# Kernel tuning notes

Hardware: AMD Instinct MI355X
Metric: run time of the kernel (lower is better)

## Reference

```python
import jax, jax.numpy as jnp
import numpy as np

G = 8            # group_order
KS = 3           # kernel size
C1, O1 = 1, 16   # gconv1 channels
C2, O2 = 16, 32  # gconv2 channels
HW = 28
NUM_CLASSES = 10


def _bilinear_sample(img, px, py):
    # img: (O, I, K, K); px, py: (K, K) pixel coords; zero padding outside
    # (matches torch grid_sample bilinear, align_corners=False, padding_mode='zeros')
    K = img.shape[-1]
    x0 = jnp.floor(px); y0 = jnp.floor(py)
    wx = px - x0; wy = py - y0
    x0i = x0.astype(jnp.int32); y0i = y0.astype(jnp.int32)

    def gather(yi, xi):
        valid = (yi >= 0) & (yi < K) & (xi >= 0) & (xi < K)
        yc = jnp.clip(yi, 0, K - 1)
        xc = jnp.clip(xi, 0, K - 1)
        return img[:, :, yc, xc] * valid.astype(img.dtype)  # (O,I,K,K)

    return (gather(y0i, x0i) * (1 - wx) * (1 - wy)
            + gather(y0i, x0i + 1) * wx * (1 - wy)
            + gather(y0i + 1, x0i) * (1 - wx) * wy
            + gather(y0i + 1, x0i + 1) * wx * wy)


def _rotated_kernels(base, group_order):
    # Replicates F.affine_grid + F.grid_sample (align_corners=False) for each rotation k.
    K = base.shape[-1]
    coords = (2.0 * jnp.arange(K, dtype=base.dtype) + 1.0) / K - 1.0  # normalized centers
    xs, ys = jnp.meshgrid(coords, coords, indexing='xy')  # x along width, y along height

    def rot_k(k):
        theta = 2.0 * np.pi * k / group_order
        c, s = jnp.cos(theta), jnp.sin(theta)
        gx = c * xs - s * ys   # theta row [cos, -sin, 0]
        gy = s * xs + c * ys   # theta row [sin,  cos, 0]
        px = ((gx + 1.0) * K - 1.0) / 2.0  # unnormalize, align_corners=False
        py = ((gy + 1.0) * K - 1.0) / 2.0
        return _bilinear_sample(base, px, py)

    return jax.vmap(rot_k)(jnp.arange(group_order, dtype=base.dtype))  # (G,O,I,K,K)


def _conv2d(x, w, pad):
    return jax.lax.conv_general_dilated(
        x, w, window_strides=(1, 1), padding=[(pad, pad), (pad, pad)],
        dimension_numbers=('NCHW', 'OIHW', 'NCHW'))


def setup_inputs() -> dict:
    key = jax.random.key(0)
    k1, k2, k3, k4, k5 = jax.random.split(key, 5)
    x = jax.random.normal(k1, (512, C1, HW, HW), dtype=jnp.float32)
    base_weight = jax.random.normal(k2, (O1, C1, KS, KS), dtype=jnp.float32)
    w2 = jax.random.normal(k3, (O2, C2, G, KS, KS), dtype=jnp.float32) * 0.05
    fc_w = jax.random.normal(k4, (NUM_CLASSES, O2 * HW * HW), dtype=jnp.float32) * 0.01
    fc_b = jax.random.normal(k5, (NUM_CLASSES,), dtype=jnp.float32) * 0.01
    return {"x": x, "base_weight": base_weight, "w2": w2, "fc_w": fc_w, "fc_b": fc_b}


def reference(x, base_weight, w2, fc_w, fc_b):
    B = x.shape[0]
    # --- GroupConv2D: steerable rotated kernels, concat along out-channels (k-major) ---
    rk = _rotated_kernels(base_weight, G)           # (G, O1, C1, K, K)
    w1 = rk.reshape(G * O1, C1, KS, KS)
    h = _conv2d(x, w1, 1)                           # (B, G*O1, 28, 28)
    h = jax.nn.relu(h)                              # GroupReLU == plain ReLU

    # --- GroupToGroupConv: circulant structure fused into one conv ---
    # torch: out channel = g*O2 + o (cat dim=1), in channel = c*G + h_idx (view layout)
    g = jnp.arange(G)[:, None]
    hh = jnp.arange(G)[None, :]
    idx = (g - hh) % G                               # (G, G)
    Wc = w2[:, :, idx]                               # (O2, C2, G_g, G_h, K, K)
    Wbig = jnp.transpose(Wc, (2, 0, 1, 3, 4, 5)).reshape(G * O2, C2 * G, KS, KS)
    h2 = _conv2d(h, Wbig, 1)                         # (B, G*O2, 28, 28)
    h2 = jax.nn.relu(h2)

    # --- GroupPooling (mean over the *inner* factor of 8, as in the torch view) ---
    p = h2.reshape(B, (G * O2) // G, G, HW, HW).mean(axis=2)  # (B, 32, 28, 28)

    # --- fc ---
    flat = p.reshape(B, -1)
    return flat @ fc_w.T + fc_b
```

## Files before the change

### kernel.cpp

```cpp
#include <hip/hip_runtime.h>
#include <hip/hip_bf16.h>
#include <cstdint>

#define AS1 __attribute__((address_space(1)))
#define AS3 __attribute__((address_space(3)))

typedef __bf16 bf16x8 __attribute__((ext_vector_type(8)));
typedef float  f32x16 __attribute__((ext_vector_type(16)));

__device__ __forceinline__ void gld_lds16(const void* g, void* l) {
    __builtin_amdgcn_global_load_lds((const AS1 void*)g, (AS3 void*)l, 16, 0, 0);
}

__global__ void k_rot(const float* __restrict__ base, float* __restrict__ w1) {
    int m = threadIdx.x;
    int g = m >> 4, o = m & 15;
    float th = 6.28318530717958647692f * (float)g / 8.0f;
    float c = cosf(th), s = sinf(th);
    for (int i = 0; i < 3; ++i) {
        float ys = (2.0f * i + 1.0f) / 3.0f - 1.0f;
        for (int j = 0; j < 3; ++j) {
            float xs = (2.0f * j + 1.0f) / 3.0f - 1.0f;
            float gx = c * xs - s * ys;
            float gy = s * xs + c * ys;
            float px = ((gx + 1.0f) * 3.0f - 1.0f) * 0.5f;
            float py = ((gy + 1.0f) * 3.0f - 1.0f) * 0.5f;
            float x0 = floorf(px), y0 = floorf(py);
            float wx = px - x0, wy = py - y0;
            int x0i = (int)x0, y0i = (int)y0;
            auto gat = [&](int yi, int xi) -> float {
                bool v = (yi >= 0) && (yi < 3) && (xi >= 0) && (xi < 3);
                int yc = min(max(yi, 0), 2), xc = min(max(xi, 0), 2);
                return v ? base[o * 9 + yc * 3 + xc] : 0.0f;
            };
            w1[m * 9 + i * 3 + j] =
                  gat(y0i, x0i)         * (1.0f - wx) * (1.0f - wy)
                + gat(y0i, x0i + 1)     * wx          * (1.0f - wy)
                + gat(y0i + 1, x0i)     * (1.0f - wx) * wy
                + gat(y0i + 1, x0i + 1) * wx          * wy;
        }
    }
}

__global__ __launch_bounds__(256) void k_conv1(const float* __restrict__ x,
                                               const float* __restrict__ w1g,
                                               const float* __restrict__ w2,
                                               __hip_bfloat16* __restrict__ hl,
                                               __hip_bfloat16* __restrict__ A) {
    int tid = threadIdx.x;

    if (blockIdx.x < 1152) {
        int i = blockIdx.x * 256 + tid;
        int r = i / 1152, k = i - r * 1152;
        int g = r >> 5, o2 = r & 31;
        int kk = k >> 7, cch = k & 127;
        int ky = kk / 3, kx = kk - ky * 3;
        int c2 = cch >> 3, hh = cch & 7;
        int gi = (g - hh) & 7;
        float val = w2[((o2 * 16 + c2) * 8 + gi) * 9 + ky * 3 + kx];
        int half = cch >> 6, kt = cch & 63;
        int t = kk * 2 + half, ks2 = kt >> 4, hi2 = (kt >> 3) & 1, e = kt & 7;
        int mh = r >> 7, i2 = (r >> 5) & 3, row = r & 31;
        int aidx = ((((t * 2 + mh) * 16) + i2 * 4 + ks2) << 9) + ((hi2 << 5) + row) * 8 + e;
        A[aidx] = __float2bfloat16(val);
    }

    __shared__ float w1s[1152];
    for (int i = tid; i < 1152; i += 256) w1s[i] = w1g[i];
    __syncthreads();

    const int c0 = (tid & 15) * 8;
    float wreg[8][9];
#pragma unroll
    for (int cc = 0; cc < 8; ++cc)
#pragma unroll
        for (int k = 0; k < 9; ++k) wreg[cc][k] = w1s[(c0 + cc) * 9 + k];

    const int slot = tid >> 4;
    const int band = blockIdx.x % 15;
    const int b    = blockIdx.x / 15;
    const int yy   = band * 2 + (slot >> 3);
    const int xx0  = (slot & 7) * 4;

    const float* xb = x + b * 784;
    float xv[3][6];
#pragma unroll
    for (int t = 0; t < 3; ++t) {
        int sy = yy - 2 + t;
        bool syok = (sy >= 0) && (sy < 28);
#pragma unroll
        for (int u = 0; u < 6; ++u) {
            int sx = xx0 - 2 + u;
            bool ok = syok && (sx >= 0) && (sx < 28);
            xv[t][u] = ok ? xb[sy * 28 + sx] : 0.0f;
        }
    }

    float acc[4][8];
#pragma unroll
    for (int j = 0; j < 4; ++j)
#pragma unroll
        for (int cc = 0; cc < 8; ++cc) acc[j][cc] = 0.0f;

#pragma unroll
    for (int t = 0; t < 3; ++t)
#pragma unroll
        for (int u = 0; u < 3; ++u) {
#pragma unroll
            for (int j = 0; j < 4; ++j) {
                float xvv = xv[t][j + u];
#pragma unroll
                for (int cc = 0; cc < 8; ++cc)
                    acc[j][cc] += xvv * wreg[cc][t * 3 + u];
            }
        }

#pragma unroll
    for (int j = 0; j < 4; ++j) {
        int xx = xx0 + j;
        if (xx < 30) {
            bool interior = (yy >= 1) && (yy <= 28) && (xx >= 1) && (xx <= 28);
            union { __hip_bfloat16 h[8]; float4 f4; } u;
#pragma unroll
            for (int cc = 0; cc < 8; ++cc)
                u.h[cc] = __float2bfloat16(interior ? fmaxf(acc[j][cc], 0.0f) : 0.0f);
            int pi = b * 900 + yy * 30 + xx;
            *(float4*)(hl + (size_t)pi * 128 + c0) = u.f4;
        }
    }
}

__global__ __launch_bounds__(512, 2) void k_conv2(const __hip_bfloat16* __restrict__ A,
                                                  const __hip_bfloat16* __restrict__ hl,
                                                  __hip_bfloat16* __restrict__ p) {
    __shared__ __align__(16) char smem[131072];

    const int tid  = threadIdx.x;
    const int lane = tid & 63;
    const int w    = tid >> 6;
    const int hi   = lane >> 5;
    const int wqr  = w >> 2;
    const int wqc  = w & 3;

    const int bid = blockIdx.x;
    const int nt  = (bid & 7) * 196 + (bid >> 3);
    const int n0  = nt << 8;

    uint32_t bSrc[2][2], ldsCh[2];
#pragma unroll
    for (int q = 0; q < 2; ++q) {
        int ch = 2 * w + q;
        int rl = ch * 8 + (lane >> 3);
        int ca = (lane & 7) ^ (rl & 7) ^ (ch & 3);
        ldsCh[q] = (uint32_t)(ch * 1024);
#pragma unroll
        for (int hn = 0; hn < 2; ++hn) {
            int n = n0 + hn * 128 + rl;
            int b = n / 784; int rr = n - b * 784;
            int y = rr / 28; int xx = rr - y * 28;
            bSrc[q][hn] = (uint32_t)(((b * 30 + y) * 30 + xx) * 256 + ca * 16);
        }
    }

    uint32_t bRd[2]; int bSw[2];
#pragma unroll
    for (int j = 0; j < 2; ++j) {
        int r = wqc * 64 + j * 32 + (lane & 31);
        bRd[j] = (uint32_t)((r >> 7) * 16384 + (r & 127) * 128);
        bSw[j] = (r & 7) ^ ((r >> 3) & 3);
    }

    const uint32_t aRd = (uint32_t)(wqr * 16384 + lane * 16);

    f32x16 acc[4][2];
#pragma unroll
    for (int i = 0; i < 4; ++i)
#pragma unroll
        for (int j = 0; j < 2; ++j) acc[i][j] = (f32x16)(0.0f);

    const char* Ab = (const char*)A;
    const char* Hb = (const char*)hl;

    auto stage = [&](int tt, char* dst) {
#pragma unroll
        for (int q = 0; q < 4; ++q)
            gld_lds16(Ab + (size_t)tt * 32768 + q * 8192 + tid * 16,
                      dst + q * 8192 + tid * 16);
        int kk = tt >> 1, half = tt & 1;
        int ky = kk / 3, kx = kk - ky * 3;
        uint32_t boff = (uint32_t)((ky * 30 + kx) * 256 + half * 128);
        gld_lds16(Hb + bSrc[0][0] + boff, dst + 32768 + ldsCh[0]);
        gld_lds16(Hb + bSrc[1][0] + boff, dst + 32768 + ldsCh[1]);
        gld_lds16(Hb + bSrc[0][1] + boff, dst + 49152 + ldsCh[0]);
        gld_lds16(Hb + bSrc[1][1] + boff, dst + 49152 + ldsCh[1]);
    };

    stage(0, smem);

#pragma unroll 1
    for (int t = 0; t < 18; ++t) {
        __syncthreads();
        char* cur = smem + ((t & 1) << 16);
        const char* LA = cur + aRd;
        const char* LB = cur + 32768;
        if (t < 17) stage(t + 1, smem + (((t + 1) & 1) << 16));

        bf16x8 aF[2][4], bF[2][2];
#pragma unroll
        for (int i = 0; i < 4; ++i)
            aF[0][i] = *(const bf16x8*)(LA + ((i * 4 + 0) << 10));
#pragma unroll
        for (int j = 0; j < 2; ++j)
            bF[0][j] = *(const bf16x8*)(LB + bRd[j] + ((uint32_t)((0 + hi) ^ bSw[j]) << 4));

#pragma unroll
        for (int ks = 0; ks < 4; ++ks) {
            const int c = ks & 1, nx = c ^ 1;
            if (ks < 3) {
#pragma unroll
                for (int i = 0; i < 4; ++i)
                    aF[nx][i] = *(const bf16x8*)(LA + ((i * 4 + ks + 1) << 10));
#pragma unroll
                for (int j = 0; j < 2; ++j)
                    bF[nx][j] = *(const bf16x8*)(LB + bRd[j] + ((uint32_t)(((ks + 1) * 2 + hi) ^ bSw[j]) << 4));
            }
#pragma unroll
            for (int i = 0; i < 4; ++i)
#pragma unroll
                for (int j = 0; j < 2; ++j)
                    acc[i][j] = __builtin_amdgcn_mfma_f32_32x32x16_bf16(aF[c][i], bF[c][j], acc[i][j], 0, 0, 0);
        }
    }

#pragma unroll
    for (int i = 0; i < 4; ++i) {
#pragma unroll
        for (int j = 0; j < 2; ++j) {
            f32x16 v = acc[i][j];
#pragma unroll
            for (int u = 0; u < 4; ++u) {
                float sv = fmaxf(v[4*u], 0.0f) + fmaxf(v[4*u+1], 0.0f)
                         + fmaxf(v[4*u+2], 0.0f) + fmaxf(v[4*u+3], 0.0f);
                sv += __shfl_xor(sv, 32, 64);
                if (hi == 0) {
                    int a = wqr * 16 + i * 4 + u;
                    int n = n0 + wqc * 64 + j * 32 + (lane & 31);
                    int b = n / 784; int rr = n - b * 784;
                    p[(b * 32 + a) * 784 + rr] = __float2bfloat16(sv * 0.125f);
                }
            }
        }
    }
}

__global__ __launch_bounds__(256) void k_fc(const __hip_bfloat16* __restrict__ p,
                                            const float* __restrict__ fw,
                                            const float* __restrict__ fb,
                                            float* __restrict__ out) {
    int b = blockIdx.x >> 2, ks = blockIdx.x & 3;
    int tid = threadIdx.x;
    const bf16x8* pb = (const bf16x8*)(p + (size_t)b * 25088);
    const float4* w4 = (const float4*)fw;
    float acc[10] = {};
    for (int t = ks * 784 + tid; t < (ks + 1) * 784; t += 256) {
        union { bf16x8 v; __hip_bfloat16 h[8]; } u;
        u.v = pb[t];
        float vf[8];
#pragma unroll
        for (int e = 0; e < 8; ++e) vf[e] = __bfloat162float(u.h[e]);
#pragma unroll
        for (int c = 0; c < 10; ++c) {
            float4 u0 = w4[c * 6272 + 2 * t];
            float4 u1 = w4[c * 6272 + 2 * t + 1];
            acc[c] += vf[0] * u0.x + vf[1] * u0.y + vf[2] * u0.z + vf[3] * u0.w
                    + vf[4] * u1.x + vf[5] * u1.y + vf[6] * u1.z + vf[7] * u1.w;
        }
    }
    __shared__ float red[10][4];
    int lane = tid & 63, wv = tid >> 6;
#pragma unroll
    for (int c = 0; c < 10; ++c) {
        float s = acc[c];
#pragma unroll
        for (int o = 32; o > 0; o >>= 1) s += __shfl_down(s, o, 64);
        if (lane == 0) red[c][wv] = s;
    }
    __syncthreads();
    if (tid < 10) {
        float s = red[tid][0] + red[tid][1] + red[tid][2] + red[tid][3];
        if (ks == 0) s += fb[tid];
        atomicAdd(&out[b * 10 + tid], s);
    }
}

extern "C" void kernel_launch(void* const* d_in, const int* in_sizes, int n_in,
                              void* d_out, int out_size, void* d_ws, size_t ws_size,
                              hipStream_t stream) {
    const float* x  = (const float*)d_in[0];
    const float* bw = (const float*)d_in[1];
    const float* w2 = (const float*)d_in[2];
    const float* fw = (const float*)d_in[3];
    const float* fb = (const float*)d_in[4];
    float* out = (float*)d_out;
    char* ws = (char*)d_ws;

    float*          w1   = (float*)(ws);
    __hip_bfloat16* Amat = (__hip_bfloat16*)(ws + 4608);
    __hip_bfloat16* hl   = (__hip_bfloat16*)(ws + 594432);
    __hip_bfloat16* p    = (__hip_bfloat16*)(ws + 118563328);

    hipMemsetAsync(d_out, 0, (size_t)out_size * sizeof(float), stream);
    k_rot  <<<1,    128, 0, stream>>>(bw, w1);
    k_conv1<<<7680, 256, 0, stream>>>(x, w1, w2, hl, Amat);
    k_conv2<<<1568, 512, 0, stream>>>(Amat, hl, p);
    k_fc   <<<2048, 256, 0, stream>>>(p, fw, fb, out);
}
```

Before: 357.3 us.

## Give each wave private B tiles in LDS and read A fragments from global

```diff
diff --git a/kernel.cpp b/kernel.cpp
--- a/kernel.cpp
+++ b/kernel.cpp
@@ -139,38 +139,36 @@
     const int lane = tid & 63;
     const int w    = tid >> 6;
     const int hi   = lane >> 5;
-    const int wqr  = w >> 2;
-    const int wqc  = w & 3;
 
     const int bid = blockIdx.x;
-    const int nt  = (bid & 7) * 196 + (bid >> 3);
-    const int n0  = nt << 8;
-
-    uint32_t bSrc[2][2], ldsCh[2];
-#pragma unroll
-    for (int q = 0; q < 2; ++q) {
-        int ch = 2 * w + q;
-        int rl = ch * 8 + (lane >> 3);
-        int ca = (lane & 7) ^ (rl & 7) ^ (ch & 3);
-        ldsCh[q] = (uint32_t)(ch * 1024);
-#pragma unroll
-        for (int hn = 0; hn < 2; ++hn) {
-            int n = n0 + hn * 128 + rl;
-            int b = n / 784; int rr = n - b * 784;
-            int y = rr / 28; int xx = rr - y * 28;
-            bSrc[q][hn] = (uint32_t)(((b * 30 + y) * 30 + xx) * 256 + ca * 16);
-        }
+    const int mh  = bid & 1;
+    const int ncr = bid >> 1;
+    const int nc  = (ncr & 7) * 98 + (ncr >> 3);
+    const int n0w = nc * 512 + w * 64;
+
+    char* myLds = smem + w * 16384;
+
+    uint32_t bSrc[8];
+#pragma unroll
+    for (int q = 0; q < 8; ++q) {
+        int rl = q * 8 + (lane >> 3);
+        int ca = (lane & 7) ^ (rl & 7) ^ (q & 3);
+        int n = n0w + rl;
+        int b = n / 784; int rr = n - b * 784;
+        int y = rr / 28; int xx = rr - y * 28;
+        bSrc[q] = (uint32_t)(((b * 30 + y) * 30 + xx) * 256 + ca * 16);
     }
 
     uint32_t bRd[2]; int bSw[2];
 #pragma unroll
     for (int j = 0; j < 2; ++j) {
-        int r = wqc * 64 + j * 32 + (lane & 31);
-        bRd[j] = (uint32_t)((r >> 7) * 16384 + (r & 127) * 128);
-        bSw[j] = (r & 7) ^ ((r >> 3) & 3);
-    }
-
-    const uint32_t aRd = (uint32_t)(wqr * 16384 + lane * 16);
+        int rl = j * 32 + (lane & 31);
+        bRd[j] = (uint32_t)(rl * 128);
+        bSw[j] = (rl & 7) ^ ((rl >> 3) & 3);
+    }
+
+    const char* gA = (const char*)A + mh * 16384 + lane * 16;
+    const char* Hb = (const char*)hl;
 
     f32x16 acc[4][2];
 #pragma unroll
@@ -178,58 +176,49 @@
 #pragma unroll
         for (int j = 0; j < 2; ++j) acc[i][j] = (f32x16)(0.0f);
 
-    const char* Ab = (const char*)A;
-    const char* Hb = (const char*)hl;
-
-    auto stage = [&](int tt, char* dst) {
-#pragma unroll
-        for (int q = 0; q < 4; ++q)
-            gld_lds16(Ab + (size_t)tt * 32768 + q * 8192 + tid * 16,
-                      dst + q * 8192 + tid * 16);
+    auto stageB = [&](int tt, uint32_t dstOff) {
         int kk = tt >> 1, half = tt & 1;
         int ky = kk / 3, kx = kk - ky * 3;
         uint32_t boff = (uint32_t)((ky * 30 + kx) * 256 + half * 128);
-        gld_lds16(Hb + bSrc[0][0] + boff, dst + 32768 + ldsCh[0]);
-        gld_lds16(Hb + bSrc[1][0] + boff, dst + 32768 + ldsCh[1]);
-        gld_lds16(Hb + bSrc[0][1] + boff, dst + 49152 + ldsCh[0]);
-        gld_lds16(Hb + bSrc[1][1] + boff, dst + 49152 + ldsCh[1]);
+#pragma unroll
+        for (int q = 0; q < 8; ++q)
+            gld_lds16(Hb + bSrc[q] + boff, myLds + dstOff + q * 1024);
     };
 
-    stage(0, smem);
+    stageB(0, 0);
 
 #pragma unroll 1
     for (int t = 0; t < 18; ++t) {
-        __syncthreads();
-        char* cur = smem + ((t & 1) << 16);
-        const char* LA = cur + aRd;
-        const char* LB = cur + 32768;
-        if (t < 17) stage(t + 1, smem + (((t + 1) & 1) << 16));
-
-        bf16x8 aF[2][4], bF[2][2];
-#pragma unroll
-        for (int i = 0; i < 4; ++i)
-            aF[0][i] = *(const bf16x8*)(LA + ((i * 4 + 0) << 10));
-#pragma unroll
-        for (int j = 0; j < 2; ++j)
-            bF[0][j] = *(const bf16x8*)(LB + bRd[j] + ((uint32_t)((0 + hi) ^ bSw[j]) << 4));
-
-#pragma unroll
-        for (int ks = 0; ks < 4; ++ks) {
-            const int c = ks & 1, nx = c ^ 1;
-            if (ks < 3) {
-#pragma unroll
-                for (int i = 0; i < 4; ++i)
-                    aF[nx][i] = *(const bf16x8*)(LA + ((i * 4 + ks + 1) << 10));
+        const uint32_t cur = (uint32_t)((t & 1) << 13);
+        const uint32_t nxt = cur ^ 8192u;
+        const char* gAt = gA + (size_t)t * 32768;
+
+        bf16x8 aF[4][4];
+#pragma unroll
+        for (int ks = 0; ks < 4; ++ks)
+#pragma unroll
+            for (int i = 0; i < 4; ++i)
+                aF[ks][i] = *(const bf16x8*)(gAt + ((i * 4 + ks) << 10));
+
+        asm volatile("s_waitcnt vmcnt(16)" ::: "memory");
+        __builtin_amdgcn_sched_barrier(0);
+
+        bf16x8 bF[4][2];
+#pragma unroll
+        for (int ks = 0; ks < 4; ++ks)
+#pragma unroll
+            for (int j = 0; j < 2; ++j)
+                bF[ks][j] = *(const bf16x8*)(myLds + cur + bRd[j] + ((uint32_t)((ks * 2 + hi) ^ bSw[j]) << 4));
+
+        if (t < 17) stageB(t + 1, nxt);
+
+#pragma unroll
+        for (int ks = 0; ks < 4; ++ks)
+#pragma unroll
+            for (int i = 0; i < 4; ++i)
 #pragma unroll
                 for (int j = 0; j < 2; ++j)
-                    bF[nx][j] = *(const bf16x8*)(LB + bRd[j] + ((uint32_t)(((ks + 1) * 2 + hi) ^ bSw[j]) << 4));
-            }
-#pragma unroll
-            for (int i = 0; i < 4; ++i)
-#pragma unroll
-                for (int j = 0; j < 2; ++j)
-                    acc[i][j] = __builtin_amdgcn_mfma_f32_32x32x16_bf16(aF[c][i], bF[c][j], acc[i][j], 0, 0, 0);
-        }
+                    acc[i][j] = __builtin_amdgcn_mfma_f32_32x32x16_bf16(aF[ks][i], bF[ks][j], acc[i][j], 0, 0, 0);
     }
 
 #pragma unroll
@@ -243,8 +232,8 @@
                          + fmaxf(v[4*u+2], 0.0f) + fmaxf(v[4*u+3], 0.0f);
                 sv += __shfl_xor(sv, 32, 64);
                 if (hi == 0) {
-                    int a = wqr * 16 + i * 4 + u;
-                    int n = n0 + wqc * 64 + j * 32 + (lane & 31);
+                    int a = mh * 16 + i * 4 + u;
+                    int n = nc * 512 + w * 64 + j * 32 + (lane & 31);
                     int b = n / 784; int rr = n - b * 784;
                     p[(b * 32 + a) * 784 + rr] = __float2bfloat16(sv * 0.125f);
                 }
```

Measured after the change: 449.1 us. 25.7% more time.
